# Performance work log

Measured on AMD Instinct MI355X. Metric: run time of the kernel, lower is better.

The kernel has to match this reference:

```python
import jax, jax.numpy as jnp
import numpy as np
from jax import lax

# Dense emulation of the irregular graph stage (repo helpers img2graph /
# IrregularMaxPool2d / GraphConv2d): nodes = pixels of the stride-4 grid.
# Where pooling_mask==1, a 2x2 block is max-pooled (pooled value replicated
# over the block) and subsequent GraphConv2d gathers neighbors with offset 2
# (dilation 2); where mask==0 the node keeps resolution and offset 1.


def _conv(x, w, b, dil=1):
    p = dil  # SAME padding for a 3x3 kernel with dilation `dil`
    y = lax.conv_general_dilated(x, w, (1, 1), ((p, p), (p, p)),
                                 rhs_dilation=(dil, dil),
                                 dimension_numbers=('NCHW', 'OIHW', 'NCHW'))
    return y + b[None, :, None, None]


def _maxpool2(x):
    return lax.reduce_window(x, -jnp.inf, lax.max, (1, 1, 2, 2), (1, 1, 2, 2), 'VALID')


def _up2(x):
    return jnp.repeat(jnp.repeat(x, 2, axis=2), 2, axis=3)


def setup_inputs() -> dict:
    key = jax.random.key(0)
    ks = jax.random.split(key, 12)
    B, H, W = 4, 384, 384
    inp = {
        'batch': jax.random.normal(ks[0], (B, 3, H, W), jnp.float32),
        'pooling_mask': jax.random.randint(ks[1], (B, 1, H // 8, W // 8), 0, 2, jnp.int32),
    }
    cfg = [(3, 64), (64, 64), (64, 128), (128, 128), (128, 256),
           (256, 256), (256, 256), (256, 512), (512, 512), (512, 512)]
    for i, (cin, cout) in enumerate(cfg):
        scale = float(np.sqrt(2.0 / (cin * 9)))  # He init for 3x3 conv
        inp[f'W{i+1}'] = jax.random.normal(ks[2 + (i % 10)], (cout, cin, 3, 3), jnp.float32) * scale
        inp[f'b{i+1}'] = jnp.zeros((cout,), jnp.float32)
    return inp


def reference(batch, pooling_mask, W1, b1, W2, b2, W3, b3, W4, b4, W5, b5,
              W6, b6, W7, b7, W8, b8, W9, b9, W10, b10):
    x = jax.nn.relu(_conv(batch, W1, b1))
    x = jax.nn.relu(_conv(x, W2, b2))
    x = _maxpool2(x)                                  # H/2
    x = jax.nn.relu(_conv(x, W3, b3))
    x = jax.nn.relu(_conv(x, W4, b4))
    x = _maxpool2(x)                                  # H/4 (OS4)
    x = jax.nn.relu(_conv(x, W5, b5))
    x = jax.nn.relu(_conv(x, W6, b6))
    x = jax.nn.relu(_conv(x, W7, b7))
    # img2graph + IrregularMaxPool2d (number_pools=1)
    m = (pooling_mask > 0).astype(x.dtype)            # [B,1,H/8,W/8]
    m_up = _up2(m)                                    # [B,1,H/4,W/4]
    x = m_up * _up2(_maxpool2(x)) + (1.0 - m_up) * x  # pool 2x2 where mask==1

    # GraphConv2d: per-node neighbor offset = 1 + mask (spatially varying dilation)
    def gconv(h, w, b):
        return m_up * _conv(h, w, b, dil=2) + (1.0 - m_up) * _conv(h, w, b, dil=1)

    x = jax.nn.relu(gconv(x, W8, b8))
    x = jax.nn.relu(gconv(x, W9, b9))
    x = jax.nn.relu(gconv(x, W10, b10))               # use_relu=True
    return x  # graph2img: nodes already laid out on the stride-4 grid
```

## Files before the change

kernel.cpp:

```cpp
#include <hip/hip_runtime.h>


typedef __attribute__((ext_vector_type(8))) short short8;
typedef __attribute__((ext_vector_type(4))) float f32x4;

__device__ __forceinline__ float b2f(ushort u) {
    return __uint_as_float(((unsigned)u) << 16);
}
__device__ __forceinline__ ushort f2b(float f) {
    unsigned x = __float_as_uint(f);
    x += 0x7FFFu + ((x >> 16) & 1u);
    return (ushort)(x >> 16);
}
__device__ __forceinline__ ushort bmax(ushort a, ushort b) {
    return b2f(a) > b2f(b) ? a : b;
}
__device__ __forceinline__ float fmaxf2(float a, float b) { return a > b ? a : b; }

struct RepackArgs {
    const float* w[9];
    ushort*      wp[9];
    int cin[9];
    int cout[9];
    int off[10];
};

__global__ __launch_bounds__(256)
void repack_all(RepackArgs a)
{
    int i = blockIdx.x * 256 + threadIdx.x;
    if (i >= a.off[9]) return;
    int l = 0;
    #pragma unroll
    for (int k = 1; k < 9; ++k) l += (i >= a.off[k]);
    int j = i - a.off[l];
    int Cin = a.cin[l], Cout = a.cout[l];
    int CBl  = Cin / 32;
    int c8   = j & 7;
    int co   = (j >> 3) % Cout;
    int rest = (j >> 3) / Cout;
    int q    = rest & 3;
    int cbt  = rest >> 2;
    int cb   = cbt % CBl;
    int t    = cbt / CBl;
    int ci   = cb * 32 + q * 8 + c8;
    a.wp[l][j] = f2b(a.w[l][((size_t)co * Cin + ci) * 9 + t]);
}

__global__ __launch_bounds__(256)
void l1_conv(const float* __restrict__ in, const float* __restrict__ w,
             const float* __restrict__ bias, ushort* __restrict__ out)
{
    const int H = 384, W = 384;
    __shared__ float s[3][18][18];
    const int tid = threadIdx.x;
    const int tilesX = W / 16;
    const int x0 = (blockIdx.x % tilesX) * 16;
    const int y0 = (blockIdx.x / tilesX) * 16;
    const int b  = blockIdx.z;

    for (int i = tid; i < 3 * 18 * 18; i += 256) {
        int ci = i / (18 * 18);
        int r  = i % (18 * 18);
        int iy = r / 18, ix = r % 18;
        int gy = y0 - 1 + iy, gx = x0 - 1 + ix;
        float v = 0.f;
        if ((unsigned)gy < (unsigned)H && (unsigned)gx < (unsigned)W)
            v = in[((size_t)(b * 3 + ci) * H + gy) * W + gx];
        s[ci][iy][ix] = v;
    }
    __syncthreads();

    const int tx = tid & 15, ty = tid >> 4;
    float iv[3][3][3];
    #pragma unroll
    for (int ci = 0; ci < 3; ++ci)
        #pragma unroll
        for (int ky = 0; ky < 3; ++ky)
            #pragma unroll
            for (int kx = 0; kx < 3; ++kx)
                iv[ci][ky][kx] = s[ci][ty + ky][tx + kx];

    size_t pix = ((size_t)(b * H + y0 + ty) * W + x0 + tx);
    #pragma unroll
    for (int c4 = 0; c4 < 4; ++c4) {
        __align__(16) ushort ob[16];
        #pragma unroll
        for (int co = 0; co < 16; ++co) {
            int coG = c4 * 16 + co;
            float a = bias[coG];
            #pragma unroll
            for (int ci = 0; ci < 3; ++ci)
                #pragma unroll
                for (int ky = 0; ky < 3; ++ky)
                    #pragma unroll
                    for (int kx = 0; kx < 3; ++kx)
                        a = fmaf(w[((size_t)coG * 3 + ci) * 9 + ky * 3 + kx],
                                 iv[ci][ky][kx], a);
            a = a > 0.f ? a : 0.f;
            ob[co] = f2b(a);
        }
        *(short8*)&out[pix * 64 + c4 * 16]     = *(short8*)&ob[0];
        *(short8*)&out[pix * 64 + c4 * 16 + 8] = *(short8*)&ob[8];
    }
}

template<int TR, int BN, int CIN, int COUT, int H, int W, bool GCONV, bool FINAL,
         int POOL>
__global__ __launch_bounds__(256)
void conv_mfma(const ushort* __restrict__ in, const ushort* __restrict__ wp,
               const float* __restrict__ bias, void* __restrict__ outv,
               const int* __restrict__ mask)
{
    constexpr int BM   = TR * 16;
    constexpr int CB   = CIN / 32;
    constexpr int HA   = GCONV ? 2 : 1;
    constexpr int CW   = 16 + 2 * HA;
    constexpr int CR   = TR + 2 * HA;
    constexpr int NCH  = CR * CW;
    constexpr int NCHP = NCH + 2;
    constexpr int WM   = BM / 64;
    constexpr int NSA  = NCH * 4;
    constexpr int NSLA = (NSA + 255) / 256;
    constexpr int NSB  = 12 * BN;
    constexpr int NSLB = NSB / 256;
    static_assert(NSB % 256 == 0, "B staging must tile 256 threads");

    __shared__ __align__(16) ushort sA[4 * NCHP * 8];
    __shared__ __align__(16) ushort sB[12 * BN * 8];

    const int tid  = threadIdx.x;
    const int lane = tid & 63;
    const int wv   = tid >> 6;
    const int wm   = wv % WM;
    const int wn   = wv / WM;
    const int col  = lane & 15;
    const int quad = lane >> 4;

    const int tiles_x = W / 16, tiles_y = H / TR;
    int sp = blockIdx.x;
    const int b  = sp / (tiles_x * tiles_y);
    int rr = sp - b * tiles_x * tiles_y;
    const int ty = rr / tiles_x;
    const int tx = rr - ty * tiles_x;
    const int y0 = ty * TR, x0 = tx * 16;
    const int co0 = blockIdx.y * BN;

    int dA[4], aoff[4];
    #pragma unroll
    for (int mt = 0; mt < 4; ++mt) {
        dA[mt] = 1;
        if (GCONV) {
            int y = y0 + wm * 4 + mt, x = x0 + col;
            dA[mt] = mask[(b * (H / 2) + (y >> 1)) * (W / 2) + (x >> 1)] ? 2 : 1;
        }
        aoff[mt] = (HA + wm * 4 + mt) * CW + HA + col;
    }

    short8 pA[NSLA];
    short8 pB[NSLB];

    auto loadA = [&](int cb) {
        #pragma unroll
        for (int k = 0; k < NSLA; ++k) {
            int i = tid + k * 256;
            short8 v = {0, 0, 0, 0, 0, 0, 0, 0};
            if (NSA == NSLA * 256 || i < NSA) {
                int chunk = i >> 2, part = i & 3;
                int yy = chunk / CW, xx = chunk - yy * CW;
                int gy = y0 - HA + yy, gx = x0 - HA + xx;
                if ((unsigned)gy < (unsigned)H && (unsigned)gx < (unsigned)W)
                    v = *(const short8*)(in + ((size_t)(b * H + gy) * W + gx) * CIN
                                         + cb * 32 + part * 8);
            }
            pA[k] = v;
        }
    };
    auto storeA = [&]() {
        #pragma unroll
        for (int k = 0; k < NSLA; ++k) {
            int i = tid + k * 256;
            if (NSA == NSLA * 256 || i < NSA) {
                int chunk = i >> 2, part = i & 3;
                *(short8*)&sA[(part * NCHP + chunk) * 8] = pA[k];
            }
        }
    };
    auto loadB = [&](int s) {
        int cb = s / 3, row = s % 3;
        #pragma unroll
        for (int k = 0; k < NSLB; ++k) {
            int i = tid + k * 256;
            int co = i % BN;
            int rq = i / BN;
            const ushort* gp = wp
                + (((size_t)(row * 3 + (rq >> 2)) * CB + cb) * 4 + (rq & 3))
                      * COUT * 8
                + (size_t)(co0 + co) * 8;
            pB[k] = *(const short8*)gp;
        }
    };
    auto storeB = [&]() {
        #pragma unroll
        for (int k = 0; k < NSLB; ++k) {
            int i = tid + k * 256;
            *(short8*)&sB[(size_t)i * 8] = pB[k];
        }
    };

    f32x4 acc[4][4];
    #pragma unroll
    for (int i = 0; i < 4; ++i)
        #pragma unroll
        for (int j = 0; j < 4; ++j)
            acc[i][j] = (f32x4){0.f, 0.f, 0.f, 0.f};

    loadA(0);
    loadB(0);
    storeA();
    storeB();
    __syncthreads();

    for (int s = 0; s < 3 * CB; ++s) {
        const int row  = s % 3;
        const bool last = (s == 3 * CB - 1);
        if (!last) {
            loadB(s + 1);
            if (row == 2) loadA(s / 3 + 1);
        }
        const int ky = row - 1;
        #pragma unroll
        for (int j = 0; j < 3; ++j) {
            const int kx = j - 1;
            short8 af[4], bf4[4];
            #pragma unroll
            for (int i = 0; i < 4; ++i) {
                int chunk = aoff[i] + dA[i] * (ky * CW + kx);
                af[i]  = *(const short8*)&sA[(quad * NCHP + chunk) * 8];
                bf4[i] = *(const short8*)&sB[((j * 4 + quad) * BN
                                              + wn * 64 + i * 16 + col) * 8];
            }
            #pragma unroll
            for (int mt = 0; mt < 4; ++mt)
                #pragma unroll
                for (int nt = 0; nt < 4; ++nt)
                    acc[mt][nt] = __builtin_amdgcn_mfma_f32_16x16x32_bf16(
                        af[mt], bf4[nt], acc[mt][nt], 0, 0, 0);
        }
        if (!last) {
            __syncthreads();
            storeB();
            if (row == 2) storeA();
            __syncthreads();
        }
    }

    if (FINAL) {
        float* outp = (float*)outv;
        #pragma unroll
        for (int mt = 0; mt < 4; ++mt) {
            int y = y0 + wm * 4 + mt;
            #pragma unroll
            for (int nt = 0; nt < 4; ++nt) {
                int co = co0 + wn * 64 + nt * 16 + col;
                float bv = bias[co];
                f32x4 vv;
                #pragma unroll
                for (int r2 = 0; r2 < 4; ++r2) {
                    float z = acc[mt][nt][r2] + bv;
                    vv[r2] = z > 0.f ? z : 0.f;
                }
                *(f32x4*)&outp[((size_t)(b * COUT + co) * H + y) * W + x0 + quad * 4] = vv;
            }
        }
    } else if (POOL == 0) {
        ushort* outp = (ushort*)outv;
        #pragma unroll
        for (int mt = 0; mt < 4; ++mt) {
            int y = y0 + wm * 4 + mt;
            #pragma unroll
            for (int nt = 0; nt < 4; ++nt) {
                int co = co0 + wn * 64 + nt * 16 + col;
                float bv = bias[co];
                #pragma unroll
                for (int r2 = 0; r2 < 4; ++r2) {
                    int x = x0 + quad * 4 + r2;
                    float vv = acc[mt][nt][r2] + bv;
                    vv = vv > 0.f ? vv : 0.f;
                    outp[((size_t)(b * H + y) * W + x) * COUT + co] = f2b(vv);
                }
            }
        }
    } else if (POOL == 1) {
        ushort* outp = (ushort*)outv;
        #pragma unroll
        for (int nt = 0; nt < 4; ++nt) {
            int co = co0 + wn * 64 + nt * 16 + col;
            float bv = bias[co];
            float v[4][4];
            #pragma unroll
            for (int mt = 0; mt < 4; ++mt)
                #pragma unroll
                for (int r2 = 0; r2 < 4; ++r2) {
                    float z = acc[mt][nt][r2] + bv;
                    v[mt][r2] = z > 0.f ? z : 0.f;
                }
            #pragma unroll
            for (int mt2 = 0; mt2 < 2; ++mt2) {
                int yp = (y0 >> 1) + wm * 2 + mt2;
                #pragma unroll
                for (int j = 0; j < 2; ++j) {
                    int xp = (x0 >> 1) + quad * 2 + j;
                    float m = fmaxf2(fmaxf2(v[2*mt2][2*j],   v[2*mt2][2*j+1]),
                                     fmaxf2(v[2*mt2+1][2*j], v[2*mt2+1][2*j+1]));
                    outp[((size_t)(b * (H/2) + yp) * (W/2) + xp) * COUT + co] = f2b(m);
                }
            }
        }
    } else {
        ushort* outp = (ushort*)outv;
        int mc[2][2];
        #pragma unroll
        for (int my = 0; my < 2; ++my)
            #pragma unroll
            for (int mx = 0; mx < 2; ++mx) {
                int y = y0 + wm * 4 + my * 2;
                int x = x0 + quad * 4 + mx * 2;
                mc[my][mx] = mask[(b * (H / 2) + (y >> 1)) * (W / 2) + (x >> 1)];
            }
        #pragma unroll
        for (int nt = 0; nt < 4; ++nt) {
            int co = co0 + wn * 64 + nt * 16 + col;
            float bv = bias[co];
            float v[4][4];
            #pragma unroll
            for (int mt = 0; mt < 4; ++mt)
                #pragma unroll
                for (int r2 = 0; r2 < 4; ++r2) {
                    float z = acc[mt][nt][r2] + bv;
                    v[mt][r2] = z > 0.f ? z : 0.f;
                }
            #pragma unroll
            for (int mt = 0; mt < 4; ++mt) {
                int y = y0 + wm * 4 + mt;
                #pragma unroll
                for (int r2 = 0; r2 < 4; ++r2) {
                    int x = x0 + quad * 4 + r2;
                    float p = fmaxf2(fmaxf2(v[mt][r2],     v[mt][r2 ^ 1]),
                                     fmaxf2(v[mt ^ 1][r2], v[mt ^ 1][r2 ^ 1]));
                    float o = mc[mt >> 1][r2 >> 1] ? p : v[mt][r2];
                    outp[((size_t)(b * H + y) * W + x) * COUT + co] = f2b(o);
                }
            }
        }
    }
}

extern "C" void kernel_launch(void* const* d_in, const int* in_sizes, int n_in,
                              void* d_out, int out_size, void* d_ws, size_t ws_size,
                              hipStream_t stream)
{
    const float* x    = (const float*)d_in[0];
    const int*   mask = (const int*)d_in[1];
    const float* Wt[10];
    const float* bs[10];
    for (int i = 0; i < 10; ++i) {
        Wt[i] = (const float*)d_in[2 + 2 * i];
        bs[i] = (const float*)d_in[3 + 2 * i];
    }

    const size_t ACT = (size_t)4 * 384 * 384 * 64;
    ushort* A  = (ushort*)d_ws;
    ushort* Bb = A + ACT;
    ushort* wpbase = Bb + ACT;

    static const int cins[10]  = {3, 64, 64, 128, 128, 256, 256, 256, 512, 512};
    static const int couts[10] = {64, 64, 128, 128, 256, 256, 256, 512, 512, 512};
    ushort* wp[10];
    size_t wo = 0;
    for (int l = 1; l < 10; ++l) {
        wp[l] = wpbase + wo;
        wo += (size_t)couts[l] * cins[l] * 9;
    }

    RepackArgs ra;
    int off = 0;
    for (int l = 1; l < 10; ++l) {
        ra.w[l - 1]    = Wt[l];
        ra.wp[l - 1]   = wp[l];
        ra.cin[l - 1]  = cins[l];
        ra.cout[l - 1] = couts[l];
        ra.off[l - 1]  = off;
        off += couts[l] * cins[l] * 9;
    }
    ra.off[9] = off;
    repack_all<<<(off + 255) / 256, 256, 0, stream>>>(ra);

    l1_conv<<<dim3(24 * 24, 1, 4), 256, 0, stream>>>(x, Wt[0], bs[0], A);

    conv_mfma<16, 64, 64, 64, 384, 384, false, false, 1>
        <<<dim3(4 * 24 * 24, 1), 256, 0, stream>>>(A, wp[1], bs[1], Bb, nullptr);

    conv_mfma<8, 128, 64, 128, 192, 192, false, false, 0>
        <<<dim3(4 * 24 * 12, 1), 256, 0, stream>>>(Bb, wp[2], bs[2], A, nullptr);
    conv_mfma<8, 128, 128, 128, 192, 192, false, false, 1>
        <<<dim3(4 * 24 * 12, 1), 256, 0, stream>>>(A, wp[3], bs[3], Bb, nullptr);

    conv_mfma<8, 128, 128, 256, 96, 96, false, false, 0>
        <<<dim3(4 * 12 * 6, 2), 256, 0, stream>>>(Bb, wp[4], bs[4], A, nullptr);
    conv_mfma<8, 128, 256, 256, 96, 96, false, false, 0>
        <<<dim3(4 * 12 * 6, 2), 256, 0, stream>>>(A, wp[5], bs[5], Bb, nullptr);
    conv_mfma<8, 128, 256, 256, 96, 96, false, false, 2>
        <<<dim3(4 * 12 * 6, 2), 256, 0, stream>>>(Bb, wp[6], bs[6], A, mask);

    conv_mfma<8, 128, 256, 512, 96, 96, true, false, 0>
        <<<dim3(4 * 12 * 6, 4), 256, 0, stream>>>(A, wp[7], bs[7], Bb, mask);
    conv_mfma<8, 128, 512, 512, 96, 96, true, false, 0>
        <<<dim3(4 * 12 * 6, 4), 256, 0, stream>>>(Bb, wp[8], bs[8], A, mask);
    conv_mfma<8, 128, 512, 512, 96, 96, true, true, 0>
        <<<dim3(4 * 12 * 6, 4), 256, 0, stream>>>(A, wp[9], bs[9], d_out, mask);

    (void)in_sizes; (void)n_in; (void)out_size; (void)ws_size;
}
```

Before: 899.7 us.

## Stage conv tiles via direct global-to-LDS loads with double-buffered shared memory

Replaces the register-staged global→register→LDS copies with global_load_lds direct transfers into double-buffered A and B shared tiles. An XOR swizzle on the A tile layout avoids bank conflicts, and out-of-bounds halo loads point at a zero pad buffer initialised in the repack kernel. The main loop is unrolled by two input-channel blocks to alternate buffers, cutting one barrier per step. LDS usage roughly doubles, which may reduce occupancy, and correctness relies on the swizzle and buffer parity being consistent.

Measured after the change: 1.112 ms. +23.6%, slower.

```diff
diff --git a/kernel.cpp b/kernel.cpp
--- a/kernel.cpp
+++ b/kernel.cpp
@@ -12,14 +12,18 @@
     x += 0x7FFFu + ((x >> 16) & 1u);
     return (ushort)(x >> 16);
 }
-__device__ __forceinline__ ushort bmax(ushort a, ushort b) {
-    return b2f(a) > b2f(b) ? a : b;
-}
 __device__ __forceinline__ float fmaxf2(float a, float b) { return a > b ? a : b; }
+
+__device__ __forceinline__ void glds16(const ushort* g, ushort* l) {
+    __builtin_amdgcn_global_load_lds(
+        (const __attribute__((address_space(1))) unsigned int*)g,
+        (__attribute__((address_space(3))) unsigned int*)l, 16, 0, 0);
+}
 
 struct RepackArgs {
     const float* w[9];
     ushort*      wp[9];
+    ushort*      zpad;
     int cin[9];
     int cout[9];
     int off[10];
@@ -28,6 +32,7 @@
 __global__ __launch_bounds__(256)
 void repack_all(RepackArgs a)
 {
+    if (blockIdx.x == 0 && threadIdx.x < 128) a.zpad[threadIdx.x] = 0;
     int i = blockIdx.x * 256 + threadIdx.x;
     if (i >= a.off[9]) return;
     int l = 0;
@@ -110,24 +115,27 @@
 __global__ __launch_bounds__(256)
 void conv_mfma(const ushort* __restrict__ in, const ushort* __restrict__ wp,
                const float* __restrict__ bias, void* __restrict__ outv,
-               const int* __restrict__ mask)
+               const int* __restrict__ mask, const ushort* __restrict__ zpad)
 {
     constexpr int BM   = TR * 16;
     constexpr int CB   = CIN / 32;
+    static_assert(CB % 2 == 0, "parity unroll needs even CB");
     constexpr int HA   = GCONV ? 2 : 1;
     constexpr int CW   = 16 + 2 * HA;
     constexpr int CR   = TR + 2 * HA;
     constexpr int NCH  = CR * CW;
-    constexpr int NCHP = NCH + 2;
     constexpr int WM   = BM / 64;
     constexpr int NSA  = NCH * 4;
-    constexpr int NSLA = (NSA + 255) / 256;
+    constexpr int NSAP = (NSA + 63) & ~63;
+    constexpr int NKA  = (NSAP + 255) / 256;
     constexpr int NSB  = 12 * BN;
     constexpr int NSLB = NSB / 256;
     static_assert(NSB % 256 == 0, "B staging must tile 256 threads");
 
-    __shared__ __align__(16) ushort sA[4 * NCHP * 8];
-    __shared__ __align__(16) ushort sB[12 * BN * 8];
+    __shared__ __align__(16) ushort sA0[NSAP * 8];
+    __shared__ __align__(16) ushort sA1[NSAP * 8];
+    __shared__ __align__(16) ushort sB0[NSB * 8];
+    __shared__ __align__(16) ushort sB1[NSB * 8];
 
     const int tid  = threadIdx.x;
     const int lane = tid & 63;
@@ -157,37 +165,25 @@
         aoff[mt] = (HA + wm * 4 + mt) * CW + HA + col;
     }
 
-    short8 pA[NSLA];
-    short8 pB[NSLB];
-
-    auto loadA = [&](int cb) {
-        #pragma unroll
-        for (int k = 0; k < NSLA; ++k) {
+    auto gldsA = [&](int cb, ushort* dst) {
+        #pragma unroll
+        for (int k = 0; k < NKA; ++k) {
             int i = tid + k * 256;
-            short8 v = {0, 0, 0, 0, 0, 0, 0, 0};
-            if (NSA == NSLA * 256 || i < NSA) {
-                int chunk = i >> 2, part = i & 3;
-                int yy = chunk / CW, xx = chunk - yy * CW;
+            if (k * 256 + (tid & ~63) < NSAP) {
+                int b2 = (i >> 2) & 1, b3 = (i >> 3) & 1, b4 = (i >> 4) & 1;
+                int r  = i ^ ((b2 ^ b4) | (b3 << 1) | (b4 << 2));
+                int ch = r >> 2, part = r & 3;
+                int yy = ch / CW, xx = ch - yy * CW;
                 int gy = y0 - HA + yy, gx = x0 - HA + xx;
-                if ((unsigned)gy < (unsigned)H && (unsigned)gx < (unsigned)W)
-                    v = *(const short8*)(in + ((size_t)(b * H + gy) * W + gx) * CIN
-                                         + cb * 32 + part * 8);
-            }
-            pA[k] = v;
+                const ushort* gp = zpad;
+                if (ch < NCH && (unsigned)gy < (unsigned)H && (unsigned)gx < (unsigned)W)
+                    gp = in + ((size_t)(b * H + gy) * W + gx) * CIN
+                            + cb * 32 + part * 8;
+                glds16(gp, dst + (size_t)i * 8);
+            }
         }
     };
-    auto storeA = [&]() {
-        #pragma unroll
-        for (int k = 0; k < NSLA; ++k) {
-            int i = tid + k * 256;
-            if (NSA == NSLA * 256 || i < NSA) {
-                int chunk = i >> 2, part = i & 3;
-                *(short8*)&sA[(part * NCHP + chunk) * 8] = pA[k];
-            }
-        }
-    };
-    auto loadB = [&](int s) {
-        int cb = s / 3, row = s % 3;
+    auto gldsB = [&](int cb, int row, ushort* dst) {
         #pragma unroll
         for (int k = 0; k < NSLB; ++k) {
             int i = tid + k * 256;
@@ -197,14 +193,7 @@
                 + (((size_t)(row * 3 + (rq >> 2)) * CB + cb) * 4 + (rq & 3))
                       * COUT * 8
                 + (size_t)(co0 + co) * 8;
-            pB[k] = *(const short8*)gp;
-        }
-    };
-    auto storeB = [&]() {
-        #pragma unroll
-        for (int k = 0; k < NSLB; ++k) {
-            int i = tid + k * 256;
-            *(short8*)&sB[(size_t)i * 8] = pB[k];
+            glds16(gp, dst + (size_t)i * 8);
         }
     };
 
@@ -215,42 +204,49 @@
         for (int j = 0; j < 4; ++j)
             acc[i][j] = (f32x4){0.f, 0.f, 0.f, 0.f};
 
-    loadA(0);
-    loadB(0);
-    storeA();
-    storeB();
+    gldsA(0, sA0);
+    gldsB(0, 0, sB0);
     __syncthreads();
 
-    for (int s = 0; s < 3 * CB; ++s) {
-        const int row  = s % 3;
-        const bool last = (s == 3 * CB - 1);
-        if (!last) {
-            loadB(s + 1);
-            if (row == 2) loadA(s / 3 + 1);
-        }
-        const int ky = row - 1;
-        #pragma unroll
-        for (int j = 0; j < 3; ++j) {
-            const int kx = j - 1;
-            short8 af[4], bf4[4];
-            #pragma unroll
-            for (int i = 0; i < 4; ++i) {
-                int chunk = aoff[i] + dA[i] * (ky * CW + kx);
-                af[i]  = *(const short8*)&sA[(quad * NCHP + chunk) * 8];
-                bf4[i] = *(const short8*)&sB[((j * 4 + quad) * BN
-                                              + wn * 64 + i * 16 + col) * 8];
-            }
-            #pragma unroll
-            for (int mt = 0; mt < 4; ++mt)
-                #pragma unroll
-                for (int nt = 0; nt < 4; ++nt)
-                    acc[mt][nt] = __builtin_amdgcn_mfma_f32_16x16x32_bf16(
-                        af[mt], bf4[nt], acc[mt][nt], 0, 0, 0);
-        }
-        if (!last) {
-            __syncthreads();
-            storeB();
-            if (row == 2) storeA();
+    for (int cb2 = 0; cb2 < CB; cb2 += 2) {
+        #pragma unroll
+        for (int t = 0; t < 6; ++t) {
+            const int row = t % 3;
+            ushort*       sBnxt = (t & 1) ? sB0 : sB1;
+            const ushort* sBcur = (t & 1) ? sB1 : sB0;
+            const ushort* sAcur = (t >= 3) ? sA1 : sA0;
+            ushort*       sAnxt = (t >= 3) ? sA0 : sA1;
+            const bool lastS = (cb2 + 2 >= CB) && (t == 5);
+            if (!lastS) {
+                int cbB  = cb2 + (t + 1) / 3;
+                int rowB = (t + 1) % 3;
+                if (t == 5) { cbB = cb2 + 2; rowB = 0; }
+                gldsB(cbB, rowB, sBnxt);
+            }
+            if (row == 2) {
+                int cbn = cb2 + (t / 3) + 1;
+                if (cbn < CB) gldsA(cbn, sAnxt);
+            }
+            const int ky = row - 1;
+            #pragma unroll
+            for (int j = 0; j < 3; ++j) {
+                const int kx = j - 1;
+                short8 af[4], bf4[4];
+                #pragma unroll
+                for (int i = 0; i < 4; ++i) {
+                    int ch = aoff[i] + dA[i] * (ky * CW + kx);
+                    int su = (ch * 4 + quad) ^ (ch & 7);
+                    af[i]  = *(const short8*)&sAcur[su * 8];
+                    bf4[i] = *(const short8*)&sBcur[((j * 4 + quad) * BN
+                                                     + wn * 64 + i * 16 + col) * 8];
+                }
+                #pragma unroll
+                for (int mt = 0; mt < 4; ++mt)
+                    #pragma unroll
+                    for (int nt = 0; nt < 4; ++nt)
+                        acc[mt][nt] = __builtin_amdgcn_mfma_f32_16x16x32_bf16(
+                            af[mt], bf4[nt], acc[mt][nt], 0, 0, 0);
+            }
             __syncthreads();
         }
     }
@@ -382,6 +378,7 @@
         wp[l] = wpbase + wo;
         wo += (size_t)couts[l] * cins[l] * 9;
     }
+    ushort* zpad = wpbase + ((wo + 7) & ~(size_t)7);
 
     RepackArgs ra;
     int off = 0;
@@ -394,31 +391,32 @@
         off += couts[l] * cins[l] * 9;
     }
     ra.off[9] = off;
+    ra.zpad = zpad;
     repack_all<<<(off + 255) / 256, 256, 0, stream>>>(ra);
 
     l1_conv<<<dim3(24 * 24, 1, 4), 256, 0, stream>>>(x, Wt[0], bs[0], A);
 
     conv_mfma<16, 64, 64, 64, 384, 384, false, false, 1>
-        <<<dim3(4 * 24 * 24, 1), 256, 0, stream>>>(A, wp[1], bs[1], Bb, nullptr);
+        <<<dim3(4 * 24 * 24, 1), 256, 0, stream>>>(A, wp[1], bs[1], Bb, nullptr, zpad);
 
     conv_mfma<8, 128, 64, 128, 192, 192, false, false, 0>
-        <<<dim3(4 * 24 * 12, 1), 256, 0, stream>>>(Bb, wp[2], bs[2], A, nullptr);
+        <<<dim3(4 * 24 * 12, 1), 256, 0, stream>>>(Bb, wp[2], bs[2], A, nullptr, zpad);
     conv_mfma<8, 128, 128, 128, 192, 192, false, false, 1>
-        <<<dim3(4 * 24 * 12, 1), 256, 0, stream>>>(A, wp[3], bs[3], Bb, nullptr);
+        <<<dim3(4 * 24 * 12, 1), 256, 0, stream>>>(A, wp[3], bs[3], Bb, nullptr, zpad);
 
     conv_mfma<8, 128, 128, 256, 96, 96, false, false, 0>
-        <<<dim3(4 * 12 * 6, 2), 256, 0, stream>>>(Bb, wp[4], bs[4], A, nullptr);
+        <<<dim3(4 * 12 * 6, 2), 256, 0, stream>>>(Bb, wp[4], bs[4], A, nullptr, zpad);
     conv_mfma<8, 128, 256, 256, 96, 96, false, false, 0>
-        <<<dim3(4 * 12 * 6, 2), 256, 0, stream>>>(A, wp[5], bs[5], Bb, nullptr);
+        <<<dim3(4 * 12 * 6, 2), 256, 0, stream>>>(A, wp[5], bs[5], Bb, nullptr, zpad);
     conv_mfma<8, 128, 256, 256, 96, 96, false, false, 2>
-        <<<dim3(4 * 12 * 6, 2), 256, 0, stream>>>(Bb, wp[6], bs[6], A, mask);
+        <<<dim3(4 * 12 * 6, 2), 256, 0, stream>>>(Bb, wp[6], bs[6], A, mask, zpad);
 
     conv_mfma<8, 128, 256, 512, 96, 96, true, false, 0>
-        <<<dim3(4 * 12 * 6, 4), 256, 0, stream>>>(A, wp[7], bs[7], Bb, mask);
+        <<<dim3(4 * 12 * 6, 4), 256, 0, stream>>>(A, wp[7], bs[7], Bb, mask, zpad);
     conv_mfma<8, 128, 512, 512, 96, 96, true, false, 0>
-        <<<dim3(4 * 12 * 6, 4), 256, 0, stream>>>(Bb, wp[8], bs[8], A, mask);
+        <<<dim3(4 * 12 * 6, 4), 256, 0, stream>>>(Bb, wp[8], bs[8], A, mask, zpad);
     conv_mfma<8, 128, 512, 512, 96, 96, true, true, 0>
-        <<<dim3(4 * 12 * 6, 4), 256, 0, stream>>>(A, wp[9], bs[9], d_out, mask);
+        <<<dim3(4 * 12 * 6, 4), 256, 0, stream>>>(A, wp[9], bs[9], d_out, mask, zpad);
 
     (void)in_sizes; (void)n_in; (void)out_size; (void)ws_size;
 }
```
